# Kernel tuning notes

Measured on AMD Instinct MI355X. Metric: run time of the kernel, lower is better.

The kernel has to match this reference:

```python
import jax, jax.numpy as jnp
import numpy as np
from jax import lax

EPS = 1e-3  # Keras LayerNormalization default epsilon

def _layernorm(x, g, b):
    m = jnp.mean(x, axis=-1, keepdims=True)
    v = jnp.var(x, axis=-1, keepdims=True)
    return (x - m) * lax.rsqrt(v + EPS) * g + b

def _conv1d_same(x, w, b, stride):
    # x: (B, T, Cin), w: (K, Cin, Cout) -> (B, ceil(T/stride), Cout), TF 'same' padding
    y = lax.conv_general_dilated(x, w, window_strides=(stride,), padding='SAME',
                                 dimension_numbers=('NWC', 'WIO', 'NWC'))
    return y + b

def _process(x, conv1_w, conv1_b, ln1_g, ln1_b, conv2_w, conv2_b, ln2_g, ln2_b):
    # SmallConvNet (dropout omitted for deterministic reference)
    x = _conv1d_same(x, conv1_w, conv1_b, 3)
    x = jax.nn.silu(_layernorm(x, ln1_g, ln1_b))
    x = _conv1d_same(x, conv2_w, conv2_b, 5)
    x = jax.nn.silu(_layernorm(x, ln2_g, ln2_b))
    return x

def setup_inputs() -> dict:
    key = jax.random.key(0)
    ks = jax.random.split(key, 4)
    B, T, E = 4, 1920, 512
    return {
        'values':  jax.random.normal(ks[0], (B, T, E), jnp.float32),
        'symbols': jax.random.normal(ks[1], (T, E), jnp.float32),
        'conv1_w': jax.random.normal(ks[2], (5, E, 128), jnp.float32) * 0.05,
        'conv1_b': jnp.zeros((128,), jnp.float32),
        'ln1_g':   jnp.ones((128,), jnp.float32),
        'ln1_b':   jnp.zeros((128,), jnp.float32),
        'conv2_w': jax.random.normal(ks[3], (3, 128, 1024), jnp.float32) * 0.05,
        'conv2_b': jnp.zeros((1024,), jnp.float32),
        'ln2_g':   jnp.ones((1024,), jnp.float32),
        'ln2_b':   jnp.zeros((1024,), jnp.float32),
    }

def reference(values, symbols, conv1_w, conv1_b, ln1_g, ln1_b, conv2_w, conv2_b, ln2_g, ln2_b):
    proc = lambda x: _process(x, conv1_w, conv1_b, ln1_g, ln1_b, conv2_w, conv2_b, ln2_g, ln2_b)
    values_projected = proc(values)                                     # (B, n, d)
    symbol_projected = proc(jnp.broadcast_to(symbols, values.shape))    # (B, n, d)
    # symbolic=True: sign-cosine similarity of X_i vs (X_i + C_j)
    a = values_projected[:, None, :, :]                                 # (B, 1, n, d) -> i on axis 2
    b = a + symbol_projected[:, :, None, :]                             # (B, n, n, d) -> j on axis 1
    S = jnp.mean(jnp.sign(a) * jnp.sign(b), axis=-1)                    # (B, n, n)
    scores = jax.nn.softmax(S, axis=-1)
    attention_output = jnp.einsum('bji,bid->bjd', scores, values_projected)
    O = jax.nn.silu(attention_output * symbol_projected)
    return (O, values_projected)
```

## Files before the change

### kernel.cpp

```cpp
#include <hip/hip_runtime.h>
#include <math.h>

#define LN_EPS 1e-3f

typedef __attribute__((ext_vector_type(8))) short short8;
typedef __attribute__((ext_vector_type(4))) float floatx4;

__device__ __forceinline__ float silu_f(float x) { return x / (1.f + expf(-x)); }

__device__ __forceinline__ int mism1(float a, float s) {
    unsigned ua = __float_as_uint(a);
    unsigned ub = __float_as_uint(a + s);
    return (int)((ua ^ ub) >> 31);
}

__device__ __forceinline__ short f2bf(float f) {
    unsigned u = __float_as_uint(f);
    unsigned r = (u + 0x7FFFu + ((u >> 16) & 1u)) >> 16;
    return (short)r;
}

__global__ __launch_bounds__(256) void k_prep(
    const float* __restrict__ w1,
    const float* __restrict__ w2,
    short* __restrict__ w1s,
    short* __restrict__ w2s)
{
    int tid = blockIdx.x * 256 + threadIdx.x;
    if (tid < 327680) {
        int j    = tid & 7;
        int lane = (tid >> 3) & 63;
        int nt   = (tid >> 9) & 7;
        int ks   = (tid >> 12) % 10;
        int kc   = tid / 40960;
        int kw = ks >> 1;
        int ci = kc * 64 + (ks & 1) * 32 + ((lane >> 4) & 3) * 8 + j;
        int n  = nt * 16 + (lane & 15);
        w1s[tid] = f2bf(w1[((size_t)(kw * 512 + ci)) * 128 + n]);
    } else {
        int t = tid - 327680;
        if (t < 393216) {
            int j    = t & 7;
            int lane = (t >> 3) & 63;
            int nt   = (t >> 9) & 63;
            int ks   = t >> 15;
            int k  = ks * 32 + ((lane >> 4) & 3) * 8 + j;
            int kw = k >> 7;
            int ci = k & 127;
            int n  = nt * 16 + (lane & 15);
            w2s[t] = f2bf(w2[((size_t)(kw * 128 + ci)) * 1024 + n]);
        }
    }
}

__global__ __launch_bounds__(512) void k_conv1m(
    const float* __restrict__ values,
    const float* __restrict__ symbols,
    const short* __restrict__ w1s,
    const float* __restrict__ b1,
    const float* __restrict__ g1,
    const float* __restrict__ bt1,
    short* __restrict__ h1)
{
    int mt  = blockIdx.x;
    int seq = mt / 40;
    int tl  = mt % 40;
    const float* x = (seq < 4) ? (values + (size_t)seq * 1920 * 512) : symbols;
    int p0 = 48 * tl - 1;

    __shared__ short xs[50 * 520];
    __shared__ float red[8][4][4][2];

    int tid  = threadIdx.x;
    int lane = tid & 63, w = tid >> 6;
    int quad = lane >> 4, mrow = lane & 15;

    for (int idx = tid; idx < 6400; idx += 512) {
        int r = idx >> 7, g = idx & 127;
        int gp = p0 + r;
        float4 v = make_float4(0.f, 0.f, 0.f, 0.f);
        if (gp >= 0 && gp < 1920)
            v = *(const float4*)(x + (size_t)gp * 512 + 4 * g);
        short4 pk;
        pk.x = f2bf(v.x); pk.y = f2bf(v.y); pk.z = f2bf(v.z); pk.w = f2bf(v.w);
        *(short4*)(xs + r * 520 + 4 * g) = pk;
    }
    __syncthreads();

    floatx4 acc = (floatx4){0.f, 0.f, 0.f, 0.f};
    for (int kc = 0; kc < 8; kc++) {
        #pragma unroll
        for (int ks = 0; ks < 10; ks++) {
            int kw  = ks >> 1;
            int ci  = kc * 64 + (ks & 1) * 32 + quad * 8;
            short8 a = *(const short8*)(xs + (3 * mrow + kw) * 520 + ci);
            short8 b = *(const short8*)(w1s +
                (((size_t)(kc * 10 + ks) * 8 + w) * 64 + lane) * 8);
            acc = __builtin_amdgcn_mfma_f32_16x16x32_bf16(a, b, acc, 0, 0, 0);
        }
    }

    int co = w * 16 + mrow;
    float b1v = b1[co], g1v = g1[co], btv = bt1[co];

    float s1[4], s2[4];
    #pragma unroll
    for (int r = 0; r < 4; r++) {
        float v = acc[r] + b1v;
        acc[r] = v;
        s1[r] = v; s2[r] = v * v;
    }
    #pragma unroll
    for (int m = 8; m >= 1; m >>= 1) {
        #pragma unroll
        for (int r = 0; r < 4; r++) {
            s1[r] += __shfl_xor(s1[r], m, 64);
            s2[r] += __shfl_xor(s2[r], m, 64);
        }
    }
    if (mrow == 0) {
        #pragma unroll
        for (int r = 0; r < 4; r++) { red[w][quad][r][0] = s1[r]; red[w][quad][r][1] = s2[r]; }
    }
    __syncthreads();

    #pragma unroll
    for (int r = 0; r < 4; r++) {
        float S1 = 0.f, S2 = 0.f;
        #pragma unroll
        for (int ww = 0; ww < 8; ww++) { S1 += red[ww][quad][r][0]; S2 += red[ww][quad][r][1]; }
        float mean = S1 * (1.f / 128.f);
        float var  = S2 * (1.f / 128.f) - mean * mean;
        float rs   = rsqrtf(var + LN_EPS);
        int row = seq * 640 + tl * 16 + quad * 4 + r;
        float o = silu_f((acc[r] - mean) * rs * g1v + btv);
        h1[(size_t)row * 128 + co] = f2bf(o);
    }
}

__global__ __launch_bounds__(1024) void k_conv2m(
    const short* __restrict__ h1,
    const short* __restrict__ w2s,
    const float* __restrict__ b2,
    const float* __restrict__ g2,
    const float* __restrict__ bt2,
    float* __restrict__ vp,
    float* __restrict__ sp)
{
    int blk  = blockIdx.x;
    int pos0 = blk * 16;
    int seq  = pos0 >> 7;
    int lcl0 = pos0 & 127;
    int row0 = seq * 640 + 5 * lcl0;

    __shared__ short xa[78 * 136];
    __shared__ float red[16][4][4][2];

    int tid = threadIdx.x;
    int lane = tid & 63, w = tid >> 6;
    int quad = lane >> 4, mrow = lane & 15;

    for (int idx = tid; idx < 78 * 16; idx += 1024) {
        int r = idx >> 4, g = idx & 15;
        *(short8*)(xa + r * 136 + g * 8) =
            *(const short8*)(h1 + (size_t)(row0 + r) * 128 + g * 8);
    }
    __syncthreads();

    floatx4 acc[4];
    #pragma unroll
    for (int nt = 0; nt < 4; nt++) acc[nt] = (floatx4){0.f, 0.f, 0.f, 0.f};

    #pragma unroll
    for (int ks = 0; ks < 12; ks++) {
        int kw  = ks >> 2;
        int ci0 = (ks & 3) * 32;
        short8 a = *(const short8*)(xa + (5 * mrow + kw) * 136 + ci0 + quad * 8);
        #pragma unroll
        for (int nt = 0; nt < 4; nt++) {
            short8 b = *(const short8*)(w2s +
                (((size_t)ks * 64 + w * 4 + nt) * 64 + lane) * 8);
            acc[nt] = __builtin_amdgcn_mfma_f32_16x16x32_bf16(a, b, acc[nt], 0, 0, 0);
        }
    }

    float b2v[4], g2v[4], btv[4];
    #pragma unroll
    for (int nt = 0; nt < 4; nt++) {
        int co = w * 64 + nt * 16 + mrow;
        b2v[nt] = b2[co]; g2v[nt] = g2[co]; btv[nt] = bt2[co];
    }

    float s1[4] = {0.f, 0.f, 0.f, 0.f}, s2[4] = {0.f, 0.f, 0.f, 0.f};
    #pragma unroll
    for (int nt = 0; nt < 4; nt++)
        #pragma unroll
        for (int r = 0; r < 4; r++) {
            float v = acc[nt][r] + b2v[nt];
            acc[nt][r] = v;
            s1[r] += v; s2[r] += v * v;
        }
    #pragma unroll
    for (int m = 8; m >= 1; m >>= 1) {
        #pragma unroll
        for (int r = 0; r < 4; r++) {
            s1[r] += __shfl_xor(s1[r], m, 64);
            s2[r] += __shfl_xor(s2[r], m, 64);
        }
    }
    if (mrow == 0) {
        #pragma unroll
        for (int r = 0; r < 4; r++) { red[w][quad][r][0] = s1[r]; red[w][quad][r][1] = s2[r]; }
    }
    __syncthreads();

    float mean[4], rs[4];
    #pragma unroll
    for (int r = 0; r < 4; r++) {
        float S1 = 0.f, S2 = 0.f;
        #pragma unroll
        for (int ww = 0; ww < 16; ww++) { S1 += red[ww][quad][r][0]; S2 += red[ww][quad][r][1]; }
        mean[r] = S1 * (1.f / 1024.f);
        float var = S2 * (1.f / 1024.f) - mean[r] * mean[r];
        rs[r] = rsqrtf(var + LN_EPS);
    }

    float* obase = (pos0 < 512) ? (vp + (size_t)pos0 * 1024)
                                : (sp + (size_t)(pos0 - 512) * 1024);
    #pragma unroll
    for (int nt = 0; nt < 4; nt++) {
        int co = w * 64 + nt * 16 + mrow;
        #pragma unroll
        for (int r = 0; r < 4; r++) {
            float o = silu_f((acc[nt][r] - mean[r]) * rs[r] * g2v[nt] + btv[nt]);
            obase[((size_t)(quad * 4 + r)) * 1024 + co] = o;
        }
    }
}

__global__ __launch_bounds__(1024) void k_count(
    const float* __restrict__ vp,
    const float* __restrict__ sp,
    int* __restrict__ S_part)
{
    int b  = blockIdx.x >> 6;
    int jg = (blockIdx.x >> 3) & 7;
    int dc = blockIdx.x & 7;
    int tid = threadIdx.x;

    __shared__ float sls[8 * 260];
    __shared__ int   cnt[16][128];

    if (tid < 512) {
        int r = tid >> 5, c = tid & 31;
        float4 v = *(const float4*)(sp + (size_t)(jg * 16 + r) * 1024 + dc * 128 + 4 * c);
        int sub = c >> 2, off = (c & 3) * 4;
        *(float4*)&sls[sub * 260 + r * 16 + off] = v;
    }
    __syncthreads();

    int i = tid >> 3, sub = tid & 7;
    const float* vr = vp + ((size_t)(b * 128 + i)) * 1024 + dc * 128 + sub * 16;
    float4 v0 = *(const float4*)(vr + 0);
    float4 v1 = *(const float4*)(vr + 4);
    float4 v2 = *(const float4*)(vr + 8);
    float4 v3 = *(const float4*)(vr + 12);

    const float* sbase = &sls[sub * 260];
    #pragma unroll
    for (int j = 0; j < 16; j++) {
        const float4* srow = (const float4*)(sbase + j * 16);
        float4 s0 = srow[0], s1 = srow[1], s2 = srow[2], s3 = srow[3];
        int m = mism1(v0.x, s0.x) + mism1(v0.y, s0.y) + mism1(v0.z, s0.z) + mism1(v0.w, s0.w)
              + mism1(v1.x, s1.x) + mism1(v1.y, s1.y) + mism1(v1.z, s1.z) + mism1(v1.w, s1.w)
              + mism1(v2.x, s2.x) + mism1(v2.y, s2.y) + mism1(v2.z, s2.z) + mism1(v2.w, s2.w)
              + mism1(v3.x, s3.x) + mism1(v3.y, s3.y) + mism1(v3.z, s3.z) + mism1(v3.w, s3.w);
        m += __shfl_xor(m, 1, 64);
        m += __shfl_xor(m, 2, 64);
        m += __shfl_xor(m, 4, 64);
        if (sub == 0) cnt[j][i] = m;
    }
    __syncthreads();

    #pragma unroll
    for (int t = 0; t < 2; t++) {
        int idx = tid + t * 1024;
        int j = idx >> 7, ii = idx & 127;
        S_part[(((size_t)(b * 128 + jg * 16 + j)) * 8 + dc) * 128 + ii] = cnt[j][ii];
    }
}

__global__ __launch_bounds__(1024) void k_sein(
    const float* __restrict__ vp,
    const float* __restrict__ sp,
    const int* __restrict__ S_part,
    float* __restrict__ O)
{
    int b  = blockIdx.x >> 6;
    int jo = (blockIdx.x >> 2) & 15;
    int dq = blockIdx.x & 3;
    int tid = threadIdx.x;

    __shared__ float  sc[8][128];
    __shared__ float4 pacc[8][8][64];
    __shared__ float  reds[8][2];

    {
        int jj = tid >> 7, ii = tid & 127;
        int j  = jo * 8 + jj;
        const int* cb = S_part + ((size_t)(b * 128 + j)) * 8 * 128 + ii;
        int c = 0;
        #pragma unroll
        for (int dcc = 0; dcc < 8; dcc++) c += cb[dcc * 128];
        float e = expf(1.f - (float)c * (2.f / 1024.f));
        float t = e;
        #pragma unroll
        for (int m = 32; m >= 1; m >>= 1) t += __shfl_xor(t, m, 64);
        if ((tid & 63) == 0) reds[jj][(tid >> 6) & 1] = t;
        __syncthreads();
        float tot = reds[jj][0] + reds[jj][1];
        sc[jj][ii] = e / tot;
    }
    __syncthreads();

    if (tid < 512) {
        int ig = tid >> 6, dcol = tid & 63;
        const float* vb = vp + ((size_t)(b * 128 + ig * 16)) * 1024 + dq * 256 + 4 * dcol;
        float4 acc[8];
        #pragma unroll
        for (int jj = 0; jj < 8; jj++) acc[jj] = make_float4(0.f, 0.f, 0.f, 0.f);
        #pragma unroll 4
        for (int k = 0; k < 16; k++) {
            float4 v = *(const float4*)(vb + (size_t)k * 1024);
            #pragma unroll
            for (int jj = 0; jj < 8; jj++) {
                float s = sc[jj][ig * 16 + k];
                acc[jj].x += s * v.x; acc[jj].y += s * v.y;
                acc[jj].z += s * v.z; acc[jj].w += s * v.w;
            }
        }
        #pragma unroll
        for (int jj = 0; jj < 8; jj++) pacc[ig][jj][dcol] = acc[jj];
    }
    __syncthreads();

    if (tid < 512) {
        int jj = tid >> 6, dcol = tid & 63;
        float4 a = pacc[0][jj][dcol];
        #pragma unroll
        for (int ig = 1; ig < 8; ig++) {
            float4 p = pacc[ig][jj][dcol];
            a.x += p.x; a.y += p.y; a.z += p.z; a.w += p.w;
        }
        int j = jo * 8 + jj;
        int d = dq * 256 + 4 * dcol;
        float4 sv = *(const float4*)(sp + (size_t)j * 1024 + d);
        float4 o;
        o.x = silu_f(a.x * sv.x);
        o.y = silu_f(a.y * sv.y);
        o.z = silu_f(a.z * sv.z);
        o.w = silu_f(a.w * sv.w);
        *(float4*)(O + ((size_t)(b * 128 + j)) * 1024 + d) = o;
    }
}

extern "C" void kernel_launch(void* const* d_in, const int* in_sizes, int n_in,
                              void* d_out, int out_size, void* d_ws, size_t ws_size,
                              hipStream_t stream) {
    const float* values  = (const float*)d_in[0];
    const float* symbols = (const float*)d_in[1];
    const float* conv1_w = (const float*)d_in[2];
    const float* conv1_b = (const float*)d_in[3];
    const float* ln1_g   = (const float*)d_in[4];
    const float* ln1_b   = (const float*)d_in[5];
    const float* conv2_w = (const float*)d_in[6];
    const float* conv2_b = (const float*)d_in[7];
    const float* ln2_g   = (const float*)d_in[8];
    const float* ln2_b   = (const float*)d_in[9];

    float* out = (float*)d_out;
    float* O   = out;
    float* vp  = out + 4 * 128 * 1024;

    float* sp  = (float*)d_ws;
    short* h1  = (short*)(sp + 128 * 1024);
    short* w1s = h1 + 3200 * 128;
    short* w2s = w1s + 327680;
    int*   S_part = (int*)(w2s + 393216);

    k_prep<<<2816, 256, 0, stream>>>(conv1_w, conv2_w, w1s, w2s);
    k_conv1m<<<200, 512, 0, stream>>>(values, symbols, w1s,
                                      conv1_b, ln1_g, ln1_b, h1);
    k_conv2m<<<40, 1024, 0, stream>>>(h1, w2s, conv2_b, ln2_g, ln2_b, vp, sp);
    k_count<<<256, 1024, 0, stream>>>(vp, sp, S_part);
    k_sein<<<256, 1024, 0, stream>>>(vp, sp, S_part, O);
}
```

Measured before the change: 132.2 us.

## Fuse five kernels into one persistent megakernel with global atomic barriers

Merges weight prep, conv1, conv2, sign-count and softmax/attention into a single 256-block launch, separating phases with atomic-counter grid barriers instead of kernel boundaries. The aim is to remove launch overhead and inter-kernel gaps across five dependent small kernels. The weight-prep phase is rewritten to read float4 from the source weights and scatter to the swizzled layout. The attention phase regroups its partial sums from 8 to 4 i-groups. It relies on all 256 blocks of 1024 threads being co-resident, and the spin barrier has an iteration cap that could silently break ordering. Phases that use only 200 or 40 blocks leave the rest idle at the barriers.

Measured after the change: 211.2 us. +59.8%, slower.

```diff
diff --git a/kernel.cpp b/kernel.cpp
--- a/kernel.cpp
+++ b/kernel.cpp
@@ -2,6 +2,7 @@
 #include <math.h>
 
 #define LN_EPS 1e-3f
+#define NBLK 256
 
 typedef __attribute__((ext_vector_type(8))) short short8;
 typedef __attribute__((ext_vector_type(4))) float floatx4;
@@ -20,347 +21,374 @@
     return (short)r;
 }
 
-__global__ __launch_bounds__(256) void k_prep(
-    const float* __restrict__ w1,
-    const float* __restrict__ w2,
-    short* __restrict__ w1s,
-    short* __restrict__ w2s)
-{
-    int tid = blockIdx.x * 256 + threadIdx.x;
-    if (tid < 327680) {
-        int j    = tid & 7;
-        int lane = (tid >> 3) & 63;
-        int nt   = (tid >> 9) & 7;
-        int ks   = (tid >> 12) % 10;
-        int kc   = tid / 40960;
-        int kw = ks >> 1;
-        int ci = kc * 64 + (ks & 1) * 32 + ((lane >> 4) & 3) * 8 + j;
-        int n  = nt * 16 + (lane & 15);
-        w1s[tid] = f2bf(w1[((size_t)(kw * 512 + ci)) * 128 + n]);
-    } else {
-        int t = tid - 327680;
-        if (t < 393216) {
-            int j    = t & 7;
-            int lane = (t >> 3) & 63;
-            int nt   = (t >> 9) & 63;
-            int ks   = t >> 15;
-            int k  = ks * 32 + ((lane >> 4) & 3) * 8 + j;
-            int kw = k >> 7;
-            int ci = k & 127;
-            int n  = nt * 16 + (lane & 15);
-            w2s[t] = f2bf(w2[((size_t)(kw * 128 + ci)) * 1024 + n]);
-        }
-    }
+__device__ __forceinline__ void gbar(int* cell) {
+    __syncthreads();
+    if (threadIdx.x == 0) {
+        __threadfence();
+        atomicAdd(cell, 1);
+        int it = 0;
+        while (atomicAdd(cell, 0) < NBLK && ++it < (1 << 18))
+            __builtin_amdgcn_s_sleep(1);
+        __threadfence();
+    }
+    __syncthreads();
 }
 
-__global__ __launch_bounds__(512) void k_conv1m(
+__global__ __launch_bounds__(1024) void k_mega(
     const float* __restrict__ values,
     const float* __restrict__ symbols,
-    const short* __restrict__ w1s,
+    const float* __restrict__ w1,
     const float* __restrict__ b1,
     const float* __restrict__ g1,
     const float* __restrict__ bt1,
-    short* __restrict__ h1)
-{
-    int mt  = blockIdx.x;
-    int seq = mt / 40;
-    int tl  = mt % 40;
-    const float* x = (seq < 4) ? (values + (size_t)seq * 1920 * 512) : symbols;
-    int p0 = 48 * tl - 1;
-
-    __shared__ short xs[50 * 520];
-    __shared__ float red[8][4][4][2];
-
-    int tid  = threadIdx.x;
-    int lane = tid & 63, w = tid >> 6;
-    int quad = lane >> 4, mrow = lane & 15;
-
-    for (int idx = tid; idx < 6400; idx += 512) {
-        int r = idx >> 7, g = idx & 127;
-        int gp = p0 + r;
-        float4 v = make_float4(0.f, 0.f, 0.f, 0.f);
-        if (gp >= 0 && gp < 1920)
-            v = *(const float4*)(x + (size_t)gp * 512 + 4 * g);
-        short4 pk;
-        pk.x = f2bf(v.x); pk.y = f2bf(v.y); pk.z = f2bf(v.z); pk.w = f2bf(v.w);
-        *(short4*)(xs + r * 520 + 4 * g) = pk;
-    }
-    __syncthreads();
-
-    floatx4 acc = (floatx4){0.f, 0.f, 0.f, 0.f};
-    for (int kc = 0; kc < 8; kc++) {
-        #pragma unroll
-        for (int ks = 0; ks < 10; ks++) {
-            int kw  = ks >> 1;
-            int ci  = kc * 64 + (ks & 1) * 32 + quad * 8;
-            short8 a = *(const short8*)(xs + (3 * mrow + kw) * 520 + ci);
-            short8 b = *(const short8*)(w1s +
-                (((size_t)(kc * 10 + ks) * 8 + w) * 64 + lane) * 8);
-            acc = __builtin_amdgcn_mfma_f32_16x16x32_bf16(a, b, acc, 0, 0, 0);
-        }
-    }
-
-    int co = w * 16 + mrow;
-    float b1v = b1[co], g1v = g1[co], btv = bt1[co];
-
-    float s1[4], s2[4];
-    #pragma unroll
-    for (int r = 0; r < 4; r++) {
-        float v = acc[r] + b1v;
-        acc[r] = v;
-        s1[r] = v; s2[r] = v * v;
-    }
-    #pragma unroll
-    for (int m = 8; m >= 1; m >>= 1) {
-        #pragma unroll
-        for (int r = 0; r < 4; r++) {
-            s1[r] += __shfl_xor(s1[r], m, 64);
-            s2[r] += __shfl_xor(s2[r], m, 64);
-        }
-    }
-    if (mrow == 0) {
-        #pragma unroll
-        for (int r = 0; r < 4; r++) { red[w][quad][r][0] = s1[r]; red[w][quad][r][1] = s2[r]; }
-    }
-    __syncthreads();
-
-    #pragma unroll
-    for (int r = 0; r < 4; r++) {
-        float S1 = 0.f, S2 = 0.f;
-        #pragma unroll
-        for (int ww = 0; ww < 8; ww++) { S1 += red[ww][quad][r][0]; S2 += red[ww][quad][r][1]; }
-        float mean = S1 * (1.f / 128.f);
-        float var  = S2 * (1.f / 128.f) - mean * mean;
-        float rs   = rsqrtf(var + LN_EPS);
-        int row = seq * 640 + tl * 16 + quad * 4 + r;
-        float o = silu_f((acc[r] - mean) * rs * g1v + btv);
-        h1[(size_t)row * 128 + co] = f2bf(o);
-    }
-}
-
-__global__ __launch_bounds__(1024) void k_conv2m(
-    const short* __restrict__ h1,
-    const short* __restrict__ w2s,
+    const float* __restrict__ w2,
     const float* __restrict__ b2,
     const float* __restrict__ g2,
     const float* __restrict__ bt2,
+    short* __restrict__ w1s,
+    short* __restrict__ w2s,
+    short* __restrict__ h1,
     float* __restrict__ vp,
-    float* __restrict__ sp)
+    float* __restrict__ sp,
+    int*   __restrict__ S_part,
+    float* __restrict__ O,
+    int*   __restrict__ bar)
 {
+    __shared__ __align__(16) char smem[53248];
+
+    int tid  = threadIdx.x;
     int blk  = blockIdx.x;
-    int pos0 = blk * 16;
-    int seq  = pos0 >> 7;
-    int lcl0 = pos0 & 127;
-    int row0 = seq * 640 + 5 * lcl0;
-
-    __shared__ short xa[78 * 136];
-    __shared__ float red[16][4][4][2];
-
-    int tid = threadIdx.x;
     int lane = tid & 63, w = tid >> 6;
     int quad = lane >> 4, mrow = lane & 15;
 
-    for (int idx = tid; idx < 78 * 16; idx += 1024) {
-        int r = idx >> 4, g = idx & 15;
-        *(short8*)(xa + r * 136 + g * 8) =
-            *(const short8*)(h1 + (size_t)(row0 + r) * 128 + g * 8);
-    }
-    __syncthreads();
-
-    floatx4 acc[4];
-    #pragma unroll
-    for (int nt = 0; nt < 4; nt++) acc[nt] = (floatx4){0.f, 0.f, 0.f, 0.f};
-
-    #pragma unroll
-    for (int ks = 0; ks < 12; ks++) {
-        int kw  = ks >> 2;
-        int ci0 = (ks & 3) * 32;
-        short8 a = *(const short8*)(xa + (5 * mrow + kw) * 136 + ci0 + quad * 8);
+    {
+        int gt = blk * 1024 + tid;
+        if (gt < 81920) {
+            int p  = gt * 4;
+            int kw = p >> 16;
+            int r  = p & 65535;
+            int ci = r >> 7;
+            int n  = r & 127;
+            float4 v = *(const float4*)(w1 + p);
+            int kc = ci >> 6, c6 = ci & 63;
+            int ks = kw * 2 + (c6 >> 5);
+            int lq = (c6 >> 3) & 3, j = c6 & 7;
+            size_t base = ((((size_t)(kc * 10 + ks) * 8 + (n >> 4)) * 64)
+                           + lq * 16 + (n & 15)) * 8 + j;
+            w1s[base + 0]  = f2bf(v.x);
+            w1s[base + 8]  = f2bf(v.y);
+            w1s[base + 16] = f2bf(v.z);
+            w1s[base + 24] = f2bf(v.w);
+        } else {
+            int t = gt - 81920;
+            if (t < 98304) {
+                int p  = t * 4;
+                int kw = p >> 17;
+                int r  = p & 131071;
+                int ci = r >> 10;
+                int n  = r & 1023;
+                float4 v = *(const float4*)(w2 + p);
+                int k  = kw * 128 + ci;
+                int ks = k >> 5, k5 = k & 31;
+                int lq = k5 >> 3, j = k5 & 7;
+                size_t base = (((size_t)ks * 64 + (n >> 4)) * 64
+                               + lq * 16 + (n & 15)) * 8 + j;
+                w2s[base + 0]  = f2bf(v.x);
+                w2s[base + 8]  = f2bf(v.y);
+                w2s[base + 16] = f2bf(v.z);
+                w2s[base + 24] = f2bf(v.w);
+            }
+        }
+    }
+    gbar(bar + 0);
+
+    if (blk < 200) {
+        short* xs  = (short*)smem;
+        float* red = (float*)(smem + 52000);
+        int seq = blk / 40, tl = blk % 40;
+        const float* x = (seq < 4) ? (values + (size_t)seq * 1920 * 512) : symbols;
+        int p0 = 48 * tl - 1;
+
+        for (int idx = tid; idx < 6400; idx += 1024) {
+            int r = idx >> 7, gg = idx & 127;
+            int gp = p0 + r;
+            float4 v = make_float4(0.f, 0.f, 0.f, 0.f);
+            if (gp >= 0 && gp < 1920)
+                v = *(const float4*)(x + (size_t)gp * 512 + 4 * gg);
+            short4 pk;
+            pk.x = f2bf(v.x); pk.y = f2bf(v.y); pk.z = f2bf(v.z); pk.w = f2bf(v.w);
+            *(short4*)(xs + r * 520 + 4 * gg) = pk;
+        }
+        __syncthreads();
+
+        floatx4 acc = (floatx4){0.f, 0.f, 0.f, 0.f};
+        if (tid < 512) {
+            for (int kc = 0; kc < 8; kc++) {
+                #pragma unroll
+                for (int ks = 0; ks < 10; ks++) {
+                    int kw = ks >> 1;
+                    int ci = kc * 64 + (ks & 1) * 32 + quad * 8;
+                    short8 a = *(const short8*)(xs + (3 * mrow + kw) * 520 + ci);
+                    short8 b = *(const short8*)(w1s +
+                        (((size_t)(kc * 10 + ks) * 8 + w) * 64 + lane) * 8);
+                    acc = __builtin_amdgcn_mfma_f32_16x16x32_bf16(a, b, acc, 0, 0, 0);
+                }
+            }
+            int co = w * 16 + mrow;
+            float b1v = b1[co];
+            float s1[4], s2[4];
+            #pragma unroll
+            for (int r = 0; r < 4; r++) {
+                float v = acc[r] + b1v;
+                acc[r] = v;
+                s1[r] = v; s2[r] = v * v;
+            }
+            #pragma unroll
+            for (int m = 8; m >= 1; m >>= 1) {
+                #pragma unroll
+                for (int r = 0; r < 4; r++) {
+                    s1[r] += __shfl_xor(s1[r], m, 64);
+                    s2[r] += __shfl_xor(s2[r], m, 64);
+                }
+            }
+            if (mrow == 0) {
+                #pragma unroll
+                for (int r = 0; r < 4; r++) {
+                    red[((w * 4 + quad) * 4 + r) * 2 + 0] = s1[r];
+                    red[((w * 4 + quad) * 4 + r) * 2 + 1] = s2[r];
+                }
+            }
+        }
+        __syncthreads();
+
+        if (tid < 512) {
+            int co = w * 16 + mrow;
+            float g1v = g1[co], btv = bt1[co];
+            #pragma unroll
+            for (int r = 0; r < 4; r++) {
+                float S1 = 0.f, S2 = 0.f;
+                #pragma unroll
+                for (int ww = 0; ww < 8; ww++) {
+                    S1 += red[((ww * 4 + quad) * 4 + r) * 2 + 0];
+                    S2 += red[((ww * 4 + quad) * 4 + r) * 2 + 1];
+                }
+                float mean = S1 * (1.f / 128.f);
+                float var  = S2 * (1.f / 128.f) - mean * mean;
+                float rs   = rsqrtf(var + LN_EPS);
+                int row = seq * 640 + tl * 16 + quad * 4 + r;
+                float o = silu_f((acc[r] - mean) * rs * g1v + btv);
+                h1[(size_t)row * 128 + co] = f2bf(o);
+            }
+        }
+    }
+    gbar(bar + 1);
+
+    if (blk < 40) {
+        short* xa  = (short*)smem;
+        float* red = (float*)(smem + 21216);
+        int pos0 = blk * 16;
+        int seq  = pos0 >> 7;
+        int lcl0 = pos0 & 127;
+        int row0 = seq * 640 + 5 * lcl0;
+
+        for (int idx = tid; idx < 78 * 16; idx += 1024) {
+            int r = idx >> 4, gg = idx & 15;
+            *(short8*)(xa + r * 136 + gg * 8) =
+                *(const short8*)(h1 + (size_t)(row0 + r) * 128 + gg * 8);
+        }
+        __syncthreads();
+
+        floatx4 acc[4];
+        #pragma unroll
+        for (int nt = 0; nt < 4; nt++) acc[nt] = (floatx4){0.f, 0.f, 0.f, 0.f};
+
+        #pragma unroll
+        for (int ks = 0; ks < 12; ks++) {
+            int kw  = ks >> 2;
+            int ci0 = (ks & 3) * 32;
+            short8 a = *(const short8*)(xa + (5 * mrow + kw) * 136 + ci0 + quad * 8);
+            #pragma unroll
+            for (int nt = 0; nt < 4; nt++) {
+                short8 b = *(const short8*)(w2s +
+                    (((size_t)ks * 64 + w * 4 + nt) * 64 + lane) * 8);
+                acc[nt] = __builtin_amdgcn_mfma_f32_16x16x32_bf16(a, b, acc[nt], 0, 0, 0);
+            }
+        }
+
+        float b2v[4], g2v[4], btv[4];
         #pragma unroll
         for (int nt = 0; nt < 4; nt++) {
-            short8 b = *(const short8*)(w2s +
-                (((size_t)ks * 64 + w * 4 + nt) * 64 + lane) * 8);
-            acc[nt] = __builtin_amdgcn_mfma_f32_16x16x32_bf16(a, b, acc[nt], 0, 0, 0);
-        }
-    }
-
-    float b2v[4], g2v[4], btv[4];
-    #pragma unroll
-    for (int nt = 0; nt < 4; nt++) {
-        int co = w * 64 + nt * 16 + mrow;
-        b2v[nt] = b2[co]; g2v[nt] = g2[co]; btv[nt] = bt2[co];
-    }
-
-    float s1[4] = {0.f, 0.f, 0.f, 0.f}, s2[4] = {0.f, 0.f, 0.f, 0.f};
-    #pragma unroll
-    for (int nt = 0; nt < 4; nt++)
+            int co = w * 64 + nt * 16 + mrow;
+            b2v[nt] = b2[co]; g2v[nt] = g2[co]; btv[nt] = bt2[co];
+        }
+
+        float s1[4] = {0.f, 0.f, 0.f, 0.f}, s2[4] = {0.f, 0.f, 0.f, 0.f};
+        #pragma unroll
+        for (int nt = 0; nt < 4; nt++)
+            #pragma unroll
+            for (int r = 0; r < 4; r++) {
+                float v = acc[nt][r] + b2v[nt];
+                acc[nt][r] = v;
+                s1[r] += v; s2[r] += v * v;
+            }
+        #pragma unroll
+        for (int m = 8; m >= 1; m >>= 1) {
+            #pragma unroll
+            for (int r = 0; r < 4; r++) {
+                s1[r] += __shfl_xor(s1[r], m, 64);
+                s2[r] += __shfl_xor(s2[r], m, 64);
+            }
+        }
+        if (mrow == 0) {
+            #pragma unroll
+            for (int r = 0; r < 4; r++) {
+                red[((w * 4 + quad) * 4 + r) * 2 + 0] = s1[r];
+                red[((w * 4 + quad) * 4 + r) * 2 + 1] = s2[r];
+            }
+        }
+        __syncthreads();
+
+        float mean[4], rs[4];
         #pragma unroll
         for (int r = 0; r < 4; r++) {
-            float v = acc[nt][r] + b2v[nt];
-            acc[nt][r] = v;
-            s1[r] += v; s2[r] += v * v;
-        }
-    #pragma unroll
-    for (int m = 8; m >= 1; m >>= 1) {
-        #pragma unroll
-        for (int r = 0; r < 4; r++) {
-            s1[r] += __shfl_xor(s1[r], m, 64);
-            s2[r] += __shfl_xor(s2[r], m, 64);
-        }
-    }
-    if (mrow == 0) {
-        #pragma unroll
-        for (int r = 0; r < 4; r++) { red[w][quad][r][0] = s1[r]; red[w][quad][r][1] = s2[r]; }
-    }
-    __syncthreads();
-
-    float mean[4], rs[4];
-    #pragma unroll
-    for (int r = 0; r < 4; r++) {
-        float S1 = 0.f, S2 = 0.f;
-        #pragma unroll
-        for (int ww = 0; ww < 16; ww++) { S1 += red[ww][quad][r][0]; S2 += red[ww][quad][r][1]; }
-        mean[r] = S1 * (1.f / 1024.f);
-        float var = S2 * (1.f / 1024.f) - mean[r] * mean[r];
-        rs[r] = rsqrtf(var + LN_EPS);
-    }
-
-    float* obase = (pos0 < 512) ? (vp + (size_t)pos0 * 1024)
-                                : (sp + (size_t)(pos0 - 512) * 1024);
-    #pragma unroll
-    for (int nt = 0; nt < 4; nt++) {
-        int co = w * 64 + nt * 16 + mrow;
-        #pragma unroll
-        for (int r = 0; r < 4; r++) {
-            float o = silu_f((acc[nt][r] - mean[r]) * rs[r] * g2v[nt] + btv[nt]);
-            obase[((size_t)(quad * 4 + r)) * 1024 + co] = o;
-        }
-    }
-}
-
-__global__ __launch_bounds__(1024) void k_count(
-    const float* __restrict__ vp,
-    const float* __restrict__ sp,
-    int* __restrict__ S_part)
-{
-    int b  = blockIdx.x >> 6;
-    int jg = (blockIdx.x >> 3) & 7;
-    int dc = blockIdx.x & 7;
-    int tid = threadIdx.x;
-
-    __shared__ float sls[8 * 260];
-    __shared__ int   cnt[16][128];
-
-    if (tid < 512) {
-        int r = tid >> 5, c = tid & 31;
-        float4 v = *(const float4*)(sp + (size_t)(jg * 16 + r) * 1024 + dc * 128 + 4 * c);
-        int sub = c >> 2, off = (c & 3) * 4;
-        *(float4*)&sls[sub * 260 + r * 16 + off] = v;
-    }
-    __syncthreads();
-
-    int i = tid >> 3, sub = tid & 7;
-    const float* vr = vp + ((size_t)(b * 128 + i)) * 1024 + dc * 128 + sub * 16;
-    float4 v0 = *(const float4*)(vr + 0);
-    float4 v1 = *(const float4*)(vr + 4);
-    float4 v2 = *(const float4*)(vr + 8);
-    float4 v3 = *(const float4*)(vr + 12);
-
-    const float* sbase = &sls[sub * 260];
-    #pragma unroll
-    for (int j = 0; j < 16; j++) {
-        const float4* srow = (const float4*)(sbase + j * 16);
-        float4 s0 = srow[0], s1 = srow[1], s2 = srow[2], s3 = srow[3];
-        int m = mism1(v0.x, s0.x) + mism1(v0.y, s0.y) + mism1(v0.z, s0.z) + mism1(v0.w, s0.w)
-              + mism1(v1.x, s1.x) + mism1(v1.y, s1.y) + mism1(v1.z, s1.z) + mism1(v1.w, s1.w)
-              + mism1(v2.x, s2.x) + mism1(v2.y, s2.y) + mism1(v2.z, s2.z) + mism1(v2.w, s2.w)
-              + mism1(v3.x, s3.x) + mism1(v3.y, s3.y) + mism1(v3.z, s3.z) + mism1(v3.w, s3.w);
-        m += __shfl_xor(m, 1, 64);
-        m += __shfl_xor(m, 2, 64);
-        m += __shfl_xor(m, 4, 64);
-        if (sub == 0) cnt[j][i] = m;
-    }
-    __syncthreads();
-
-    #pragma unroll
-    for (int t = 0; t < 2; t++) {
-        int idx = tid + t * 1024;
-        int j = idx >> 7, ii = idx & 127;
-        S_part[(((size_t)(b * 128 + jg * 16 + j)) * 8 + dc) * 128 + ii] = cnt[j][ii];
-    }
-}
-
-__global__ __launch_bounds__(1024) void k_sein(
-    const float* __restrict__ vp,
-    const float* __restrict__ sp,
-    const int* __restrict__ S_part,
-    float* __restrict__ O)
-{
-    int b  = blockIdx.x >> 6;
-    int jo = (blockIdx.x >> 2) & 15;
-    int dq = blockIdx.x & 3;
-    int tid = threadIdx.x;
-
-    __shared__ float  sc[8][128];
-    __shared__ float4 pacc[8][8][64];
-    __shared__ float  reds[8][2];
+            float S1 = 0.f, S2 = 0.f;
+            #pragma unroll
+            for (int ww = 0; ww < 16; ww++) {
+                S1 += red[((ww * 4 + quad) * 4 + r) * 2 + 0];
+                S2 += red[((ww * 4 + quad) * 4 + r) * 2 + 1];
+            }
+            mean[r] = S1 * (1.f / 1024.f);
+            float var = S2 * (1.f / 1024.f) - mean[r] * mean[r];
+            rs[r] = rsqrtf(var + LN_EPS);
+        }
+
+        float* obase = (pos0 < 512) ? (vp + (size_t)pos0 * 1024)
+                                    : (sp + (size_t)(pos0 - 512) * 1024);
+        #pragma unroll
+        for (int nt = 0; nt < 4; nt++) {
+            int co = w * 64 + nt * 16 + mrow;
+            #pragma unroll
+            for (int r = 0; r < 4; r++) {
+                float o = silu_f((acc[nt][r] - mean[r]) * rs[r] * g2v[nt] + btv[nt]);
+                obase[((size_t)(quad * 4 + r)) * 1024 + co] = o;
+            }
+        }
+    }
+    gbar(bar + 2);
 
     {
-        int jj = tid >> 7, ii = tid & 127;
-        int j  = jo * 8 + jj;
-        const int* cb = S_part + ((size_t)(b * 128 + j)) * 8 * 128 + ii;
-        int c = 0;
-        #pragma unroll
-        for (int dcc = 0; dcc < 8; dcc++) c += cb[dcc * 128];
-        float e = expf(1.f - (float)c * (2.f / 1024.f));
-        float t = e;
-        #pragma unroll
-        for (int m = 32; m >= 1; m >>= 1) t += __shfl_xor(t, m, 64);
-        if ((tid & 63) == 0) reds[jj][(tid >> 6) & 1] = t;
-        __syncthreads();
-        float tot = reds[jj][0] + reds[jj][1];
-        sc[jj][ii] = e / tot;
-    }
-    __syncthreads();
-
-    if (tid < 512) {
-        int ig = tid >> 6, dcol = tid & 63;
-        const float* vb = vp + ((size_t)(b * 128 + ig * 16)) * 1024 + dq * 256 + 4 * dcol;
-        float4 acc[8];
-        #pragma unroll
-        for (int jj = 0; jj < 8; jj++) acc[jj] = make_float4(0.f, 0.f, 0.f, 0.f);
-        #pragma unroll 4
-        for (int k = 0; k < 16; k++) {
-            float4 v = *(const float4*)(vb + (size_t)k * 1024);
-            #pragma unroll
-            for (int jj = 0; jj < 8; jj++) {
-                float s = sc[jj][ig * 16 + k];
-                acc[jj].x += s * v.x; acc[jj].y += s * v.y;
-                acc[jj].z += s * v.z; acc[jj].w += s * v.w;
-            }
-        }
-        #pragma unroll
-        for (int jj = 0; jj < 8; jj++) pacc[ig][jj][dcol] = acc[jj];
-    }
-    __syncthreads();
-
-    if (tid < 512) {
-        int jj = tid >> 6, dcol = tid & 63;
-        float4 a = pacc[0][jj][dcol];
-        #pragma unroll
-        for (int ig = 1; ig < 8; ig++) {
-            float4 p = pacc[ig][jj][dcol];
-            a.x += p.x; a.y += p.y; a.z += p.z; a.w += p.w;
-        }
-        int j = jo * 8 + jj;
-        int d = dq * 256 + 4 * dcol;
-        float4 sv = *(const float4*)(sp + (size_t)j * 1024 + d);
-        float4 o;
-        o.x = silu_f(a.x * sv.x);
-        o.y = silu_f(a.y * sv.y);
-        o.z = silu_f(a.z * sv.z);
-        o.w = silu_f(a.w * sv.w);
-        *(float4*)(O + ((size_t)(b * 128 + j)) * 1024 + d) = o;
+        float* sls = (float*)smem;
+        int*   cnt = (int*)(smem + 8320);
+        int b  = blk >> 6;
+        int jg = (blk >> 3) & 7;
+        int dc = blk & 7;
+
+        if (tid < 512) {
+            int r = tid >> 5, c = tid & 31;
+            float4 v = *(const float4*)(sp + (size_t)(jg * 16 + r) * 1024 + dc * 128 + 4 * c);
+            int sub = c >> 2, off = (c & 3) * 4;
+            *(float4*)&sls[sub * 260 + r * 16 + off] = v;
+        }
+        __syncthreads();
+
+        int i = tid >> 3, sub = tid & 7;
+        const float* vr = vp + ((size_t)(b * 128 + i)) * 1024 + dc * 128 + sub * 16;
+        float4 v0 = *(const float4*)(vr + 0);
+        float4 v1 = *(const float4*)(vr + 4);
+        float4 v2 = *(const float4*)(vr + 8);
+        float4 v3 = *(const float4*)(vr + 12);
+
+        const float* sbase = &sls[sub * 260];
+        #pragma unroll
+        for (int j = 0; j < 16; j++) {
+            const float4* srow = (const float4*)(sbase + j * 16);
+            float4 s0 = srow[0], s1 = srow[1], s2 = srow[2], s3 = srow[3];
+            int m = mism1(v0.x, s0.x) + mism1(v0.y, s0.y) + mism1(v0.z, s0.z) + mism1(v0.w, s0.w)
+                  + mism1(v1.x, s1.x) + mism1(v1.y, s1.y) + mism1(v1.z, s1.z) + mism1(v1.w, s1.w)
+                  + mism1(v2.x, s2.x) + mism1(v2.y, s2.y) + mism1(v2.z, s2.z) + mism1(v2.w, s2.w)
+                  + mism1(v3.x, s3.x) + mism1(v3.y, s3.y) + mism1(v3.z, s3.z) + mism1(v3.w, s3.w);
+            m += __shfl_xor(m, 1, 64);
+            m += __shfl_xor(m, 2, 64);
+            m += __shfl_xor(m, 4, 64);
+            if (sub == 0) cnt[j * 128 + i] = m;
+        }
+        __syncthreads();
+
+        #pragma unroll
+        for (int t = 0; t < 2; t++) {
+            int idx = tid + t * 1024;
+            int j = idx >> 7, ii = idx & 127;
+            S_part[(((size_t)(b * 128 + jg * 16 + j)) * 8 + dc) * 128 + ii] = cnt[j * 128 + ii];
+        }
+    }
+    gbar(bar + 3);
+
+    {
+        float*  sc   = (float*)smem;
+        float4* pacc = (float4*)(smem + 4096);
+        float*  reds = (float*)(smem + 4096 + 32768);
+        int b  = blk >> 6;
+        int jo = (blk >> 2) & 15;
+        int dq = blk & 3;
+
+        {
+            int jj = tid >> 7, ii = tid & 127;
+            int j  = jo * 8 + jj;
+            const int* cb = S_part + ((size_t)(b * 128 + j)) * 8 * 128 + ii;
+            int c = 0;
+            #pragma unroll
+            for (int dcc = 0; dcc < 8; dcc++) c += cb[dcc * 128];
+            float e = expf(1.f - (float)c * (2.f / 1024.f));
+            float t = e;
+            #pragma unroll
+            for (int m = 32; m >= 1; m >>= 1) t += __shfl_xor(t, m, 64);
+            if ((tid & 63) == 0) reds[jj * 2 + ((tid >> 6) & 1)] = t;
+            __syncthreads();
+            float tot = reds[jj * 2 + 0] + reds[jj * 2 + 1];
+            sc[jj * 128 + ii] = e / tot;
+        }
+        __syncthreads();
+
+        if (tid < 512) {
+            int ig = tid >> 7, jh = (tid >> 6) & 1, dcol = tid & 63;
+            const float* vb = vp + ((size_t)(b * 128 + ig * 32)) * 1024 + dq * 256 + 4 * dcol;
+            float4 acc[4];
+            #pragma unroll
+            for (int jj = 0; jj < 4; jj++) acc[jj] = make_float4(0.f, 0.f, 0.f, 0.f);
+            #pragma unroll 4
+            for (int k = 0; k < 32; k++) {
+                float4 v = *(const float4*)(vb + (size_t)k * 1024);
+                #pragma unroll
+                for (int jj = 0; jj < 4; jj++) {
+                    float s = sc[(jh * 4 + jj) * 128 + ig * 32 + k];
+                    acc[jj].x += s * v.x; acc[jj].y += s * v.y;
+                    acc[jj].z += s * v.z; acc[jj].w += s * v.w;
+                }
+            }
+            #pragma unroll
+            for (int jj = 0; jj < 4; jj++)
+                pacc[(ig * 8 + jh * 4 + jj) * 64 + dcol] = acc[jj];
+        }
+        __syncthreads();
+
+        if (tid < 512) {
+            int jj = tid >> 6, dcol = tid & 63;
+            float4 a = pacc[(0 * 8 + jj) * 64 + dcol];
+            #pragma unroll
+            for (int ig = 1; ig < 4; ig++) {
+                float4 p = pacc[(ig * 8 + jj) * 64 + dcol];
+                a.x += p.x; a.y += p.y; a.z += p.z; a.w += p.w;
+            }
+            int j = jo * 8 + jj;
+            int d = dq * 256 + 4 * dcol;
+            float4 sv = *(const float4*)(sp + (size_t)j * 1024 + d);
+            float4 o;
+            o.x = silu_f(a.x * sv.x);
+            o.y = silu_f(a.y * sv.y);
+            o.z = silu_f(a.z * sv.z);
+            o.w = silu_f(a.w * sv.w);
+            *(float4*)(O + ((size_t)(b * 128 + j)) * 1024 + d) = o;
+        }
     }
 }
 
@@ -387,11 +415,12 @@
     short* w1s = h1 + 3200 * 128;
     short* w2s = w1s + 327680;
     int*   S_part = (int*)(w2s + 393216);
-
-    k_prep<<<2816, 256, 0, stream>>>(conv1_w, conv2_w, w1s, w2s);
-    k_conv1m<<<200, 512, 0, stream>>>(values, symbols, w1s,
-                                      conv1_b, ln1_g, ln1_b, h1);
-    k_conv2m<<<40, 1024, 0, stream>>>(h1, w2s, conv2_b, ln2_g, ln2_b, vp, sp);
-    k_count<<<256, 1024, 0, stream>>>(vp, sp, S_part);
-    k_sein<<<256, 1024, 0, stream>>>(vp, sp, S_part, O);
+    int*   bar    = S_part + 4 * 128 * 8 * 128;
+
+    hipMemsetAsync(bar, 0, 4 * sizeof(int), stream);
+    k_mega<<<NBLK, 1024, 0, stream>>>(
+        values, symbols,
+        conv1_w, conv1_b, ln1_g, ln1_b,
+        conv2_w, conv2_b, ln2_g, ln2_b,
+        w1s, w2s, h1, vp, sp, S_part, O, bar);
 }
```
